# Optimization experiments

Hardware: AMD Instinct MI355X
Metric: run time of the kernel (lower is better)

Reference implementation:

```python
import jax, jax.numpy as jnp
import numpy as np

N_IN = 4096      # input features
N_NPB = 64       # neurons (inputs) per branch column
N_B = 64         # branches
N_NEXT_H = 256   # next hidden width
COLS = N_B * N_NEXT_H
BATCH = 128


def setup_inputs() -> dict:
    key = jax.random.key(0)
    k1, k2, k3 = jax.random.split(key, 3)
    x = jax.random.normal(k1, (BATCH, N_IN), dtype=jnp.float32)
    # torch kaiming_normal_ on (n_npb, cols): fan_in = cols, gain = sqrt(2)
    std = np.sqrt(2.0 / COLS).astype(np.float32)
    w = jax.random.normal(k2, (N_NPB, COLS), dtype=jnp.float32) * std
    # random per-column input indices (the module's all_branch_indices)
    idx = jax.random.randint(k3, (N_NPB, COLS), 0, N_IN, dtype=jnp.int32)
    return {"x": x, "w": w, "idx": idx}


def _last_write_mask(idx):
    # (row, col) targets. keep[k, c] is True iff no k' > k has idx[k', c] == idx[k, c].
    eq = idx[:, None, :] == idx[None, :, :]                    # [K, K, C]
    later = jnp.triu(jnp.ones((N_NPB, N_NPB), bool), 1)        # k' > k
    return ~jnp.any(eq & later[:, :, None], axis=1)            # [K, C]


def reference(x, w, idx):
    keep = _last_write_mask(idx)
    w_eff = jnp.where(keep, w, jnp.zeros((), x.dtype))         # [K, C]
    cols = jnp.broadcast_to(jnp.arange(COLS), (N_NPB, COLS))
    # scatter weights into dense [n_in, cols] (equals torch's clone+index_put)
    dense = jnp.zeros((N_IN, COLS), x.dtype).at[idx, cols].add(w_eff)
    out = x @ dense                                            # [B, COLS]
    return out.reshape(-1, N_B, N_NEXT_H)
```

## Files before the change

### kernel.cpp

```cpp
#include <hip/hip_runtime.h>

#define N_IN   4096
#define N_NPB  64
#define COLS   16384
#define BATCH  128

typedef unsigned int       uint;
typedef unsigned short     ushort;
typedef __attribute__((ext_vector_type(2))) _Float16 h2;


static __device__ __forceinline__ ushort f16bits(float v) {
  return __builtin_bit_cast(ushort, (_Float16)v);
}

template <int KB>
static __device__ __forceinline__ void keep_pk(
    const int* __restrict__ ip, const float* __restrict__ wp,
    uint* __restrict__ pkout) {
  int  g[16];
  uint m[16];
#pragma unroll
  for (int j = 0; j < 16; ++j) { g[j] = ip[(KB + j) * COLS]; m[j] = 0xffffffffu; }
#pragma unroll
  for (int j = 0; j < 16; ++j)
#pragma unroll
    for (int kp = j + 1; kp < 16; ++kp)
      m[j] = min(m[j], (uint)(g[j] ^ g[kp]));
#pragma unroll 4
  for (int kp = KB + 16; kp < 64; ++kp) {
    const int vk = ip[kp * COLS];
#pragma unroll
    for (int j = 0; j < 16; ++j) m[j] = min(m[j], (uint)(g[j] ^ vk));
  }
#pragma unroll
  for (int j = 0; j < 16; ++j) {
    const float wv = (m[j] != 0u) ? wp[(KB + j) * COLS] : 0.0f;
    pkout[(KB + j) * COLS] = ((uint)g[j] << 16) | (uint)f16bits(wv);
  }
}

__global__ __launch_bounds__(256, 4) void prep_kernel(
    const float* __restrict__ x, const int* __restrict__ idx,
    const float* __restrict__ w, ushort* __restrict__ xT16,
    uint* __restrict__ pku) {
  const int bid = blockIdx.x;
  const int tid = threadIdx.x;
  if (bid < 512) {
    __shared__ float tile[32][33];
    const int i0 = (bid & 127) * 32;
    const int b0 = (bid >> 7) * 32;
    const int tx = tid & 31;
    const int ty = tid >> 5;
#pragma unroll
    for (int j = 0; j < 32; j += 8)
      tile[ty + j][tx] = x[(b0 + ty + j) * N_IN + i0 + tx];
    __syncthreads();
#pragma unroll
    for (int j = 0; j < 32; j += 8) {
      const int b = b0 + tx, i = i0 + ty + j;
      xT16[((b >> 3) << 15) + (i << 3) + (b & 7)] = f16bits(tile[tx][ty + j]);
    }
  } else {
    const int kg = __builtin_amdgcn_readfirstlane(tid >> 6);
    const int c  = (bid - 512) * 64 + (tid & 63);
    if      (kg == 0) keep_pk<0 >(idx + c, w + c, pku + c);
    else if (kg == 1) keep_pk<16>(idx + c, w + c, pku + c);
    else if (kg == 2) keep_pk<32>(idx + c, w + c, pku + c);
    else              keep_pk<48>(idx + c, w + c, pku + c);
  }
}

__global__ __launch_bounds__(512, 4) void gather_kernel(
    const uint* __restrict__ pku, const ushort* __restrict__ xT16,
    float* __restrict__ out) {
  __shared__ __align__(16) ushort xls[4096 * 8];

  const int tid  = threadIdx.x;
  const int bid  = blockIdx.x;
  const int r    = bid & 31;
  const int s    = bid >> 5;
  const int wave = tid >> 6;
  const int lane = tid & 63;
  const int c    = r * 512 + wave * 64 + lane;

  uint pk[64];
#pragma unroll
  for (int k = 0; k < 64; ++k) pk[k] = pku[k * COLS + c];

  {
    const ushort* src = xT16 + (s << 15);
#pragma unroll
    for (int t = 0; t < 8; ++t) {
      const int off = (wave * 8 + t) * 512;
      __builtin_amdgcn_global_load_lds(
          (const __attribute__((address_space(1))) void*)(src + off + lane * 8),
          (__attribute__((address_space(3))) void*)(xls + off), 16, 0, 0);
    }
  }
  __syncthreads();

  h2 a0 = (h2)0.0f, a1 = (h2)0.0f, a2 = (h2)0.0f, a3 = (h2)0.0f;
  const char* xb = (const char*)xls;
#pragma unroll
  for (int k = 0; k < 64; ++k) {
    const uint e   = pk[k];
    const uint off = (e >> 16) << 4;
    const uint wb  = e & 0xffffu;
    const h2   wh  = __builtin_bit_cast(h2, (wb << 16) | wb);
    const uint4 u  = *(const uint4*)(xb + off);
    a0 += __builtin_bit_cast(h2, u.x) * wh;
    a1 += __builtin_bit_cast(h2, u.y) * wh;
    a2 += __builtin_bit_cast(h2, u.z) * wh;
    a3 += __builtin_bit_cast(h2, u.w) * wh;
  }

  float o[8] = {(float)a0.x, (float)a0.y, (float)a1.x, (float)a1.y,
                (float)a2.x, (float)a2.y, (float)a3.x, (float)a3.y};
#pragma unroll
  for (int b = 0; b < 8; ++b)
    out[(s * 8 + b) * COLS + c] = o[b];
}

extern "C" void kernel_launch(void* const* d_in, const int* in_sizes, int n_in,
                              void* d_out, int out_size, void* d_ws, size_t ws_size,
                              hipStream_t stream) {
  const float* x   = (const float*)d_in[0];
  const float* w   = (const float*)d_in[1];
  const int*   idx = (const int*)d_in[2];
  float* out = (float*)d_out;

  char* ws = (char*)d_ws;
  ushort* xT16 = (ushort*)(ws);
  uint*   pku  = (uint*)(ws + (1u << 20));

  hipLaunchKernelGGL(prep_kernel, dim3(768), dim3(256), 0, stream,
                     x, idx, w, xT16, pku);
  hipLaunchKernelGGL(gather_kernel, dim3(512), dim3(512), 0, stream,
                     pku, xT16, out);
}
```

Baseline: 26.19 us.

## Split gather batch tile from 8 to 4 rows to double blocks and occupancy

The transposed x layout changes from groups of 8 batch rows to groups of 4, which halves the LDS tile per block (32KB to 16KB). Grid size doubles to 1024 and launch bounds allow 8 blocks per CU. Packed weights are now loaded from global memory inside the loop instead of being preloaded into 64 registers. Two k-steps run per iteration into separate accumulators that are summed at the end. The aim is higher occupancy and better latency hiding, at the cost of reading pku twice as many times overall (once per batch group).

```diff
diff --git a/kernel.cpp b/kernel.cpp
--- a/kernel.cpp
+++ b/kernel.cpp
@@ -42,7 +42,7 @@
 
 __global__ __launch_bounds__(256, 4) void prep_kernel(
     const float* __restrict__ x, const int* __restrict__ idx,
-    const float* __restrict__ w, ushort* __restrict__ xT16,
+    const float* __restrict__ w, ushort* __restrict__ xT4,
     uint* __restrict__ pku) {
   const int bid = blockIdx.x;
   const int tid = threadIdx.x;
@@ -59,7 +59,7 @@
 #pragma unroll
     for (int j = 0; j < 32; j += 8) {
       const int b = b0 + tx, i = i0 + ty + j;
-      xT16[((b >> 3) << 15) + (i << 3) + (b & 7)] = f16bits(tile[tx][ty + j]);
+      xT4[((b >> 2) << 14) + (i << 2) + (b & 3)] = f16bits(tile[tx][ty + j]);
     }
   } else {
     const int kg = __builtin_amdgcn_readfirstlane(tid >> 6);
@@ -71,10 +71,10 @@
   }
 }
 
-__global__ __launch_bounds__(512, 4) void gather_kernel(
-    const uint* __restrict__ pku, const ushort* __restrict__ xT16,
+__global__ __launch_bounds__(512, 8) void gather_kernel(
+    const uint* __restrict__ pku, const ushort* __restrict__ xT4,
     float* __restrict__ out) {
-  __shared__ __align__(16) ushort xls[4096 * 8];
+  __shared__ __align__(16) ushort xls[4096 * 4];
 
   const int tid  = threadIdx.x;
   const int bid  = blockIdx.x;
@@ -84,42 +84,42 @@
   const int lane = tid & 63;
   const int c    = r * 512 + wave * 64 + lane;
 
-  uint pk[64];
+  {
+    const ushort* src = xT4 + (s << 14);
 #pragma unroll
-  for (int k = 0; k < 64; ++k) pk[k] = pku[k * COLS + c];
-
-  {
-    const ushort* src = xT16 + (s << 15);
-#pragma unroll
-    for (int t = 0; t < 8; ++t) {
-      const int off = (wave * 8 + t) * 512;
+    for (int t = 0; t < 4; ++t) {
+      const int ub = (t * 8 + wave) * 512;
       __builtin_amdgcn_global_load_lds(
-          (const __attribute__((address_space(1))) void*)(src + off + lane * 8),
-          (__attribute__((address_space(3))) void*)(xls + off), 16, 0, 0);
+          (const __attribute__((address_space(1))) void*)(src + ub + lane * 8),
+          (__attribute__((address_space(3))) void*)(xls + ub), 16, 0, 0);
     }
   }
   __syncthreads();
 
+  const uint* pc = pku + c;
+  const char* xb = (const char*)xls;
   h2 a0 = (h2)0.0f, a1 = (h2)0.0f, a2 = (h2)0.0f, a3 = (h2)0.0f;
-  const char* xb = (const char*)xls;
 #pragma unroll
-  for (int k = 0; k < 64; ++k) {
-    const uint e   = pk[k];
-    const uint off = (e >> 16) << 4;
-    const uint wb  = e & 0xffffu;
-    const h2   wh  = __builtin_bit_cast(h2, (wb << 16) | wb);
-    const uint4 u  = *(const uint4*)(xb + off);
-    a0 += __builtin_bit_cast(h2, u.x) * wh;
-    a1 += __builtin_bit_cast(h2, u.y) * wh;
-    a2 += __builtin_bit_cast(h2, u.z) * wh;
-    a3 += __builtin_bit_cast(h2, u.w) * wh;
+  for (int k = 0; k < N_NPB; k += 2) {
+    const uint e0 = pc[k * COLS];
+    const uint e1 = pc[(k + 1) * COLS];
+    const uint o0 = (e0 >> 16) << 3;
+    const uint o1 = (e1 >> 16) << 3;
+    const uint w0 = e0 & 0xffffu, w1 = e1 & 0xffffu;
+    const h2 wh0 = __builtin_bit_cast(h2, (w0 << 16) | w0);
+    const h2 wh1 = __builtin_bit_cast(h2, (w1 << 16) | w1);
+    const uint2 u0 = *(const uint2*)(xb + o0);
+    const uint2 u1 = *(const uint2*)(xb + o1);
+    a0 += __builtin_bit_cast(h2, u0.x) * wh0;
+    a1 += __builtin_bit_cast(h2, u0.y) * wh0;
+    a2 += __builtin_bit_cast(h2, u1.x) * wh1;
+    a3 += __builtin_bit_cast(h2, u1.y) * wh1;
   }
 
-  float o[8] = {(float)a0.x, (float)a0.y, (float)a1.x, (float)a1.y,
-                (float)a2.x, (float)a2.y, (float)a3.x, (float)a3.y};
-#pragma unroll
-  for (int b = 0; b < 8; ++b)
-    out[(s * 8 + b) * COLS + c] = o[b];
+  out[(s * 4 + 0) * COLS + c] = (float)a0.x + (float)a2.x;
+  out[(s * 4 + 1) * COLS + c] = (float)a0.y + (float)a2.y;
+  out[(s * 4 + 2) * COLS + c] = (float)a1.x + (float)a3.x;
+  out[(s * 4 + 3) * COLS + c] = (float)a1.y + (float)a3.y;
 }
 
 extern "C" void kernel_launch(void* const* d_in, const int* in_sizes, int n_in,
@@ -131,11 +131,11 @@
   float* out = (float*)d_out;
 
   char* ws = (char*)d_ws;
-  ushort* xT16 = (ushort*)(ws);
-  uint*   pku  = (uint*)(ws + (1u << 20));
+  ushort* xT4 = (ushort*)(ws);
+  uint*   pku = (uint*)(ws + (1u << 20));
 
   hipLaunchKernelGGL(prep_kernel, dim3(768), dim3(256), 0, stream,
-                     x, idx, w, xT16, pku);
-  hipLaunchKernelGGL(gather_kernel, dim3(512), dim3(512), 0, stream,
-                     pku, xT16, out);
+                     x, idx, w, xT4, pku);
+  hipLaunchKernelGGL(gather_kernel, dim3(1024), dim3(512), 0, stream,
+                     pku, xT4, out);
 }
```

New measurement: 26.66 us. Within noise of the previous version (+1.8%).
